# Optimization experiments

Measured on AMD Instinct MI355X. Metric: run time of the kernel, lower is better.

## Reference

```python
import jax, jax.numpy as jnp
import numpy as np

# dims: L layers, T steps, N envs, D d_model, H heads, DH d_head, M mem_len, DI d_inner
L, T, N, D, H, DH, M, DI = 6, 128, 32, 1024, 16, 64, 128, 4096


def _layer_norm(x, g, b, eps=1e-5):
    mu = jnp.mean(x, axis=-1, keepdims=True)
    var = jnp.mean(jnp.square(x - mu), axis=-1, keepdims=True)
    return (x - mu) * jax.lax.rsqrt(var + eps) * g + b


def _rel_shift(x):
    # x: (n, h, q, k) with k axis indexed by relative distance (k-1 .. 0)
    n, h, q, k = x.shape
    x = jnp.pad(x, ((0, 0), (0, 0), (0, 0), (1, 0)))
    x = x.reshape(n, h, k + 1, q)[:, :, 1:, :].reshape(n, h, q, k)
    return x


def setup_inputs() -> dict:
    key = jax.random.key(0)
    ks = jax.random.split(key, 16)
    s = 0.02
    inp = {
        "x": jax.random.normal(ks[0], (T * N, D), jnp.float32),
        "context": jax.random.normal(ks[1], (T * N, D), jnp.float32),
        "mems": jax.random.normal(ks[2], (L, N, M, D), jnp.float32),
        "masks": jnp.ones((T * N,), jnp.float32),
        "Wq": jax.random.normal(ks[3], (L, D, H * DH), jnp.float32) * s,
        "Wk": jax.random.normal(ks[4], (L, D, H * DH), jnp.float32) * s,
        "Wv": jax.random.normal(ks[5], (L, D, H * DH), jnp.float32) * s,
        "Wr": jax.random.normal(ks[6], (L, D, H * DH), jnp.float32) * s,
        "Wo": jax.random.normal(ks[7], (L, H * DH, D), jnp.float32) * s,
        "W1": jax.random.normal(ks[8], (L, D, DI), jnp.float32) * s,
        "b1": jnp.zeros((L, DI), jnp.float32),
        "W2": jax.random.normal(ks[9], (L, DI, D), jnp.float32) * s,
        "b2": jnp.zeros((L, D), jnp.float32),
        "ln1_g": jnp.ones((L, D), jnp.float32),
        "ln1_b": jnp.zeros((L, D), jnp.float32),
        "ln2_g": jnp.ones((L, D), jnp.float32),
        "ln2_b": jnp.zeros((L, D), jnp.float32),
        "r_w_bias": jax.random.normal(ks[10], (H, DH), jnp.float32) * s,
        "r_r_bias": jax.random.normal(ks[11], (H, DH), jnp.float32) * s,
    }
    return inp


def reference(x, context, mems, masks, Wq, Wk, Wv, Wr, Wo, W1, b1, W2, b2,
              ln1_g, ln1_b, ln2_g, ln2_b, r_w_bias, r_r_bias):
    n = mems.shape[1]
    t = x.shape[0] // n
    m = mems.shape[2]
    klen = m + t
    dh = r_w_bias.shape[-1]
    h_heads = r_w_bias.shape[0]

    xs = x.reshape(t, n, -1)
    ctx = context.reshape(t, n, -1)
    mk = masks.reshape(t, n)

    # zero memories for envs that reset at the first step (mems * masks)
    mems = mems * mk[0][None, :, None, None]

    # episode-reset attention mask: token i attends token j iff j<=i and no
    # reset (mask==0) happened between them; memory visible only before any reset
    ep = jnp.cumsum((mk == 0.0).astype(jnp.int32), axis=0)  # (t, n)
    epT = ep.T  # (n, t)
    causal = jnp.tril(jnp.ones((t, t), bool))
    allow_seq = causal[None, :, :] & (epT[:, :, None] == epT[:, None, :])  # (n,t,t)
    allow_mem = jnp.broadcast_to((epT == 0)[:, :, None], (n, t, m))  # (n,t,m)
    allow = jnp.concatenate([allow_mem, allow_seq], axis=-1)[:, None]  # (n,1,t,K)

    # sinusoidal relative position embedding, distances klen-1 .. 0
    pos = jnp.arange(klen - 1, -1, -1, dtype=x.dtype)
    inv_freq = 1.0 / (10000.0 ** (jnp.arange(0, xs.shape[-1], 2, dtype=x.dtype) / xs.shape[-1]))
    ang = pos[:, None] * inv_freq[None, :]
    R = jnp.concatenate([jnp.sin(ang), jnp.cos(ang)], axis=-1)  # (K, D)

    h = xs + ctx  # fuse observation features with goal context
    scale = 1.0 / jnp.sqrt(jnp.asarray(dh, x.dtype))

    n_layer = mems.shape[0]
    for l in range(n_layer):
        cat = jnp.concatenate([jnp.transpose(mems[l], (1, 0, 2)), h], axis=0)  # (K,n,D)
        q = (h @ Wq[l]).reshape(t, n, h_heads, dh)
        k = (cat @ Wk[l]).reshape(klen, n, h_heads, dh)
        v = (cat @ Wv[l]).reshape(klen, n, h_heads, dh)
        r = (R @ Wr[l]).reshape(klen, h_heads, dh)
        AC = jnp.einsum('inhd,jnhd->nhij', q + r_w_bias, k)
        BD = _rel_shift(jnp.einsum('inhd,jhd->nhij', q + r_r_bias, r))
        score = (AC + BD) * scale
        score = jnp.where(allow, score, -1e9)
        attn = jax.nn.softmax(score, axis=-1)
        o = jnp.einsum('nhij,jnhd->inhd', attn, v).reshape(t, n, h_heads * dh) @ Wo[l]
        h = _layer_norm(h + o, ln1_g[l], ln1_b[l])
        f = jax.nn.relu(h @ W1[l] + b1[l]) @ W2[l] + b2[l]
        h = _layer_norm(h + f, ln2_g[l], ln2_b[l])

    return h.reshape(t * n, -1)
```

## Files before the change

### kernel.cpp

```cpp
#include <hip/hip_runtime.h>
#include <stdint.h>

#define DEV static __device__ __forceinline__

typedef __attribute__((ext_vector_type(4))) float f32x4;
typedef __attribute__((ext_vector_type(8))) short bf16x8;
typedef __attribute__((ext_vector_type(4))) short s16x4;

static constexpr int L_ = 6, T_ = 128, NE = 32, D_ = 1024, H_ = 16, DH_ = 64, M_ = 128, DI_ = 4096;
static constexpr int KLEN = M_ + T_;
static constexpr int TN = T_ * NE;
static constexpr int NB = NE * H_;

DEV unsigned short f2bf(float f) {
  unsigned u = __builtin_bit_cast(unsigned, f);
  u += 0x7FFFu + ((u >> 16) & 1u);
  return (unsigned short)(u >> 16);
}
DEV float bf2f(unsigned short h) {
  unsigned u = ((unsigned)h) << 16;
  return __builtin_bit_cast(float, u);
}

DEV void gload16(const unsigned short* g, unsigned short* lds) {
  __builtin_amdgcn_global_load_lds(
      (const __attribute__((address_space(1))) unsigned int*)g,
      (__attribute__((address_space(3))) unsigned int*)lds, 16, 0, 0);
}

DEV void stage128(const unsigned short* __restrict__ Ab, int lda,
                  const unsigned short* __restrict__ Bb, int ldb,
                  unsigned short* lA, unsigned short* lB,
                  int m0, int n0, int k0, int w, int l)
{
#pragma unroll
  for (int i = 0; i < 4; ++i) {
    const int obb = i * 4096 + w * 1024;
    const int ob  = obb + (l << 4);
    const int row = ob >> 7;
    const int col = (((ob >> 4) & 7) ^ (row & 7)) << 3;
    gload16(Ab + (size_t)(m0 + row) * lda + k0 + col, lA + (obb >> 1));
    gload16(Bb + (size_t)(n0 + row) * ldb + k0 + col, lB + (obb >> 1));
  }
}

DEV void compute128(const unsigned short* lA, const unsigned short* lB,
                    int w, int l, f32x4 acc[4][4])
{
  const int wr = (w >> 1) * 64, wc = (w & 1) * 64;
  const int lan = l & 15, lgr = l >> 4;
#pragma unroll
  for (int ks = 0; ks < 2; ++ks) {
    bf16x8 av[4], bv[4];
#pragma unroll
    for (int m = 0; m < 4; ++m) {
      const int row = wr + m * 16 + lan;
      const int byte = ((row << 7) + (ks << 6) + (lgr << 4)) ^ ((row & 7) << 4);
      av[m] = *(const bf16x8*)((const char*)lA + byte);
    }
#pragma unroll
    for (int n = 0; n < 4; ++n) {
      const int row = wc + n * 16 + lan;
      const int byte = ((row << 7) + (ks << 6) + (lgr << 4)) ^ ((row & 7) << 4);
      bv[n] = *(const bf16x8*)((const char*)lB + byte);
    }
#pragma unroll
    for (int m = 0; m < 4; ++m)
#pragma unroll
      for (int n = 0; n < 4; ++n)
        acc[m][n] = __builtin_amdgcn_mfma_f32_16x16x32_bf16(av[m], bv[n], acc[m][n], 0, 0, 0);
  }
}

DEV void gemm128_2ph(const unsigned short* __restrict__ Ab, int lda,
                     const unsigned short* __restrict__ Bb, int ldb,
                     unsigned short (*shA)[8192], unsigned short (*shB)[8192],
                     int m0, int n0, int nK, int w, int l, f32x4 acc[4][4])
{
  stage128(Ab, lda, Bb, ldb, shA[0], shB[0], m0, n0, 0, w, l);
  asm volatile("s_waitcnt vmcnt(0)" ::: "memory");
  __syncthreads();
  int cur = 0;
  for (int kt = 0; kt < nK; ++kt) {
    if (kt + 1 < nK)
      stage128(Ab, lda, Bb, ldb, shA[cur ^ 1], shB[cur ^ 1], m0, n0, (kt + 1) * 64, w, l);
    compute128(shA[cur], shB[cur], w, l, acc);
    asm volatile("s_waitcnt vmcnt(0)" ::: "memory");
    __syncthreads();
    cur ^= 1;
  }
}

template <int EPI>
__global__ __launch_bounds__(256) void gemm_bt(
    const unsigned short* __restrict__ A, int lda, int sAn, int sAh,
    const unsigned short* __restrict__ B, int ldb, int sBn, int sBh,
    void* __restrict__ Cv, int ldc, int sC,
    const float* __restrict__ bias, int nK, int Hb)
{
  __shared__ unsigned short shA[2][8192];
  __shared__ unsigned short shB[2][8192];

  const int z = blockIdx.z;
  const int bn = z / Hb, bh = z % Hb;
  const unsigned short* Ab = A + (size_t)bn * sAn + (size_t)bh * sAh;
  const unsigned short* Bb = B + (size_t)bn * sBn + (size_t)bh * sBh;
  const int m0 = blockIdx.y * 128;
  const int n0 = blockIdx.x * 128;

  const int t = threadIdx.x;
  const int w = t >> 6, l = t & 63;
  const int wr = (w >> 1) * 64, wc = (w & 1) * 64;
  const int lan = l & 15, lgr = l >> 4;

  f32x4 acc[4][4];
#pragma unroll
  for (int m = 0; m < 4; ++m)
#pragma unroll
    for (int n = 0; n < 4; ++n) acc[m][n] = (f32x4){0.f, 0.f, 0.f, 0.f};

  gemm128_2ph(Ab, lda, Bb, ldb, shA, shB, m0, n0, nK, w, l, acc);

  const int zc = z * sC;
#pragma unroll
  for (int m = 0; m < 4; ++m) {
    const int row = m0 + wr + m * 16 + lgr * 4;
#pragma unroll
    for (int n = 0; n < 4; ++n) {
      const int col = n0 + wc + n * 16 + lan;
      const float bcol = (EPI >= 2) ? bias[col] : 0.f;
#pragma unroll
      for (int e = 0; e < 4; ++e) {
        float v = acc[m][n][e];
        const size_t idx = (size_t)zc + (size_t)(row + e) * ldc + col;
        if (EPI == 0) {
          ((float*)Cv)[idx] = v;
        } else if (EPI == 1) {
          ((unsigned short*)Cv)[idx] = f2bf(v);
        } else if (EPI == 2) {
          v += bcol; v = v > 0.f ? v : 0.f;
          ((unsigned short*)Cv)[idx] = f2bf(v);
        } else {
          ((float*)Cv)[idx] = v + bcol;
        }
      }
    }
  }
}

__global__ __launch_bounds__(256) void gemm_proj(
    const unsigned short* __restrict__ catA, const unsigned short* __restrict__ wt,
    unsigned short* __restrict__ kb, unsigned short* __restrict__ vb,
    unsigned short* __restrict__ qw, unsigned short* __restrict__ qr,
    unsigned short* __restrict__ rb,
    const float* __restrict__ rwb, const float* __restrict__ rrb)
{
  __shared__ unsigned short shA[2][8192];
  __shared__ unsigned short shB[2][8192];

  const int id = blockIdx.x;
  int by, bx;
  if (id < 1024)      { by = id >> 4;               bx = id & 15; }
  else if (id < 1280) { const int u = id - 1024; by = 32 + (u >> 3); bx = 16 + (u & 7); }
  else                { const int u = id - 1280; by = 64 + (u >> 3); bx = 24 + (u & 7); }
  const int m0 = by * 128, n0 = bx * 128;

  const int t = threadIdx.x;
  const int w = t >> 6, l = t & 63;
  const int wr = (w >> 1) * 64, wc = (w & 1) * 64;
  const int lan = l & 15, lgr = l >> 4;

  f32x4 acc[4][4];
#pragma unroll
  for (int m = 0; m < 4; ++m)
#pragma unroll
    for (int n = 0; n < 4; ++n) acc[m][n] = (f32x4){0.f, 0.f, 0.f, 0.f};

  gemm128_2ph(catA, 1024, wt, 1024, shA, shB, m0, n0, 16, w, l, acc);

#pragma unroll
  for (int m = 0; m < 4; ++m) {
    const int row = m0 + wr + m * 16 + lgr * 4;
#pragma unroll
    for (int n = 0; n < 4; ++n) {
      const int col = n0 + wc + n * 16 + lan;
#pragma unroll
      for (int e = 0; e < 4; ++e) {
        const float v = acc[m][n][e];
        const int r = row + e;
        if (col < 1024) {
          kb[(size_t)r * 1024 + col] = f2bf(v);
        } else if (col < 2048) {
          vb[(size_t)r * 1024 + col - 1024] = f2bf(v);
        } else if (col < 3072) {
          const int c = col - 2048;
          const size_t o = (size_t)(r - 4096) * 1024 + c;
          qw[o] = f2bf(v + rwb[c]);
          qr[o] = f2bf(v + rrb[c]);
        } else {
          const int c = col - 3072;
          rb[(size_t)(r - 8192) * 1024 + c] = f2bf(v);
        }
      }
    }
  }
}

__global__ __launch_bounds__(256) void gemm_scores(
    const unsigned short* __restrict__ qw, const unsigned short* __restrict__ qr,
    const unsigned short* __restrict__ kbf, const unsigned short* __restrict__ rbf,
    unsigned short* __restrict__ AC, unsigned short* __restrict__ BD)
{
  __shared__ unsigned short shA[2][8192];
  __shared__ unsigned short shB[2][8192];

  const int bx = blockIdx.x;
  const int z = blockIdx.y;
  const int nn = z >> 4, hh = z & 15;
  const bool isBD = bx >= 2;
  const int n0 = (bx & 1) * 128;
  const unsigned short* Ab = (isBD ? qr : qw) + (size_t)nn * 1024 + hh * 64;
  const unsigned short* Bb = isBD ? (rbf + hh * 64)
                                  : (kbf + (size_t)nn * 1024 + hh * 64);
  const int ldb = isBD ? 1024 : (NE * 1024);
  unsigned short* C = (isBD ? BD : AC) + (size_t)z * (T_ * KLEN);

  const int t = threadIdx.x;
  const int w = t >> 6, l = t & 63;
  const int wr = (w >> 1) * 64, wc = (w & 1) * 64;
  const int lan = l & 15, lgr = l >> 4;

  f32x4 acc[4][4];
#pragma unroll
  for (int m = 0; m < 4; ++m)
#pragma unroll
    for (int n = 0; n < 4; ++n) acc[m][n] = (f32x4){0.f, 0.f, 0.f, 0.f};

  gemm128_2ph(Ab, NE * 1024, Bb, ldb, shA, shB, 0, n0, 1, w, l, acc);

#pragma unroll
  for (int m = 0; m < 4; ++m) {
    const int row = wr + m * 16 + lgr * 4;
#pragma unroll
    for (int n = 0; n < 4; ++n) {
      const int col = n0 + wc + n * 16 + lan;
#pragma unroll
      for (int e = 0; e < 4; ++e)
        C[(size_t)(row + e) * KLEN + col] = f2bf(acc[m][n][e]);
    }
  }
}

__global__ __launch_bounds__(256) void pv_kernel(
    const unsigned short* __restrict__ P, const unsigned short* __restrict__ V,
    unsigned short* __restrict__ O)
{
  const int z = blockIdx.x;
  const int nn = z >> 4, hh = z & 15;
  const int t = threadIdx.x, w = t >> 6, l = t & 63;
  const int lan = l & 15, lgr = l >> 4;
  const int i0 = w * 32;
  const unsigned short* Pz = P + (size_t)z * (T_ * KLEN);
  const unsigned short* Vz = V + hh * DH_;

  f32x4 acc[2][4];
#pragma unroll
  for (int m = 0; m < 2; ++m)
#pragma unroll
    for (int n = 0; n < 4; ++n) acc[m][n] = (f32x4){0.f, 0.f, 0.f, 0.f};

  for (int ks = 0; ks < 8; ++ks) {
    const int kb = ks * 32 + lgr * 8;
    bf16x8 bv[4];
#pragma unroll
    for (int n = 0; n < 4; ++n) {
      const int d = n * 16 + lan;
      bf16x8 tmp;
#pragma unroll
      for (int jj = 0; jj < 8; ++jj)
        tmp[jj] = (short)Vz[(size_t)((kb + jj) * NE + nn) * 1024 + d];
      bv[n] = tmp;
    }
    bf16x8 av[2];
#pragma unroll
    for (int m = 0; m < 2; ++m)
      av[m] = *(const bf16x8*)&Pz[(size_t)(i0 + m * 16 + lan) * KLEN + kb];
#pragma unroll
    for (int m = 0; m < 2; ++m)
#pragma unroll
      for (int n = 0; n < 4; ++n)
        acc[m][n] = __builtin_amdgcn_mfma_f32_16x16x32_bf16(av[m], bv[n], acc[m][n], 0, 0, 0);
  }
#pragma unroll
  for (int m = 0; m < 2; ++m)
#pragma unroll
    for (int n = 0; n < 4; ++n)
#pragma unroll
      for (int e = 0; e < 4; ++e) {
        const int i = i0 + m * 16 + lgr * 4 + e;
        const int d = n * 16 + lan;
        O[(size_t)(i * NE + nn) * 1024 + hh * DH_ + d] = f2bf(acc[m][n][e]);
      }
}

__global__ __launch_bounds__(256) void softmax_kernel(
    const unsigned short* __restrict__ AC, const unsigned short* __restrict__ BD,
    const int* __restrict__ ep, unsigned short* __restrict__ P)
{
  const int g = blockIdx.x * 4 + (threadIdx.x >> 6);
  const int l = threadIdx.x & 63;
  const int z = g >> 7, i = g & 127;
  const int nn = z >> 4;
  const size_t base = (size_t)z * (T_ * KLEN) + (size_t)i * KLEN;
  const int j0 = l * 4;
  const int epi = ep[i * NE + nn];
  s16x4 ac4 = *(const s16x4*)&AC[base + j0];
  float sc[4];
#pragma unroll
  for (int q = 0; q < 4; ++q) {
    const int j = j0 + q;
    int jx = j + (T_ - 1) - i; if (jx > KLEN - 1) jx = KLEN - 1;
    const float bd = bf2f((unsigned short)BD[base + jx]);
    bool allow;
    if (j < M_) {
      allow = (epi == 0);
    } else {
      const int jp = j - M_;
      allow = (jp <= i) && (ep[jp * NE + nn] == epi);
    }
    const float v = (bf2f((unsigned short)ac4[q]) + bd) * 0.125f;
    sc[q] = allow ? v : -1e9f;
  }
  float mx = fmaxf(fmaxf(sc[0], sc[1]), fmaxf(sc[2], sc[3]));
#pragma unroll
  for (int o = 32; o; o >>= 1) mx = fmaxf(mx, __shfl_xor(mx, o));
  float p[4], sum = 0.f;
#pragma unroll
  for (int q = 0; q < 4; ++q) { p[q] = __expf(sc[q] - mx); sum += p[q]; }
#pragma unroll
  for (int o = 32; o; o >>= 1) sum += __shfl_xor(sum, o);
  const float inv = 1.f / sum;
  s16x4 o4;
#pragma unroll
  for (int q = 0; q < 4; ++q) o4[q] = (short)f2bf(p[q] * inv);
  *(s16x4*)&P[base + j0] = o4;
}

__global__ __launch_bounds__(256) void transpose_kernel(
    const float* __restrict__ W, unsigned short* __restrict__ WT, int Kd, int Nd)
{
  __shared__ float tile[32][33];
  const int tx = threadIdx.x & 31, ty = threadIdx.x >> 5;
  const int nIn = blockIdx.x * 32 + tx;
  const int kBase = blockIdx.y * 32;
#pragma unroll
  for (int r = 0; r < 32; r += 8)
    tile[ty + r][tx] = W[(size_t)(kBase + ty + r) * Nd + nIn];
  __syncthreads();
#pragma unroll
  for (int r = 0; r < 32; r += 8)
    WT[(size_t)(blockIdx.x * 32 + ty + r) * Kd + kBase + tx] = f2bf(tile[tx][ty + r]);
}

__global__ __launch_bounds__(256) void catmem_kernel(
    const float* __restrict__ mems_l, const float* __restrict__ masks,
    unsigned short* __restrict__ cat)
{
  const int idx = blockIdx.x * 256 + threadIdx.x;
  const int d = idx & 1023;
  const int r = idx >> 10;
  const int nn = r & 31, j = r >> 5;
  const float mk0 = masks[nn];
  cat[idx] = f2bf(mems_l[(size_t)(nn * M_ + j) * 1024 + d] * mk0);
}

__global__ __launch_bounds__(256) void hprep_kernel(
    const float* __restrict__ x, const float* __restrict__ ctx,
    float* __restrict__ h, unsigned short* __restrict__ catUp)
{
  const int idx = blockIdx.x * 256 + threadIdx.x;
  const float v = x[idx] + ctx[idx];
  h[idx] = v;
  catUp[idx] = f2bf(v);
}

__global__ __launch_bounds__(256) void rpos_kernel(unsigned short* __restrict__ R)
{
  const int idx = blockIdx.x * 256 + threadIdx.x;
  const int d = idx & 1023, j = idx >> 10;
  const float pos = (float)(KLEN - 1 - j);
  const int f = d & 511;
  const float inv_freq = __expf(-((float)(2 * f) * (1.f / 1024.f)) * 9.210340371976184f);
  const float ang = pos * inv_freq;
  const float v = (d < 512) ? sinf(ang) : cosf(ang);
  R[idx] = f2bf(v);
}

__global__ void ep_kernel(const float* __restrict__ masks, int* __restrict__ ep)
{
  const int nn = threadIdx.x;
  if (nn < NE) {
    int c = 0;
    for (int i = 0; i < T_; ++i) {
      c += (masks[i * NE + nn] == 0.f) ? 1 : 0;
      ep[i * NE + nn] = c;
    }
  }
}

__global__ __launch_bounds__(256) void ln_kernel(
    const float* __restrict__ a, const float* __restrict__ p0,
    const float* __restrict__ p1, const float* __restrict__ bias,
    const float* __restrict__ g, const float* __restrict__ bb,
    float* __restrict__ outf, unsigned short* __restrict__ outbf)
{
  const int row = blockIdx.x;
  const int t = threadIdx.x, w = t >> 6, l = t & 63;
  const int c = t * 4;
  const size_t base = (size_t)row * 1024;
  f32x4 va = *(const f32x4*)&a[base + c];
  f32x4 v0 = *(const f32x4*)&p0[base + c];
  f32x4 v1 = *(const f32x4*)&p1[base + c];
  f32x4 v = va + v0 + v1;
  if (bias) {
    f32x4 vb = *(const f32x4*)&bias[c];
    v = v + vb;
  }
  float s = v[0] + v[1] + v[2] + v[3];
#pragma unroll
  for (int o = 32; o; o >>= 1) s += __shfl_xor(s, o);
  __shared__ float red[8];
  if (l == 0) red[w] = s;
  __syncthreads();
  s = red[0] + red[1] + red[2] + red[3];
  const float mu = s * (1.f / 1024.f);
  f32x4 dv = v - mu;
  float s2 = dv[0]*dv[0] + dv[1]*dv[1] + dv[2]*dv[2] + dv[3]*dv[3];
#pragma unroll
  for (int o = 32; o; o >>= 1) s2 += __shfl_xor(s2, o);
  if (l == 0) red[4 + w] = s2;
  __syncthreads();
  s2 = red[4] + red[5] + red[6] + red[7];
  const float inv = rsqrtf(s2 * (1.f / 1024.f) + 1e-5f);
  f32x4 y;
#pragma unroll
  for (int q = 0; q < 4; ++q) y[q] = dv[q] * inv * g[c + q] + bb[c + q];
  *(f32x4*)&outf[base + c] = y;
  if (outbf) {
    s16x4 o4;
#pragma unroll
    for (int q = 0; q < 4; ++q) o4[q] = (short)f2bf(y[q]);
    *(s16x4*)&outbf[base + c] = o4;
  }
}

extern "C" void kernel_launch(void* const* d_in, const int* in_sizes, int n_in,
                              void* d_out, int out_size, void* d_ws, size_t ws_size,
                              hipStream_t stream)
{
  (void)in_sizes; (void)n_in; (void)out_size; (void)ws_size;
  const float* x    = (const float*)d_in[0];
  const float* ctx  = (const float*)d_in[1];
  const float* mems = (const float*)d_in[2];
  const float* masks= (const float*)d_in[3];
  const float* Wq   = (const float*)d_in[4];
  const float* Wk   = (const float*)d_in[5];
  const float* Wv   = (const float*)d_in[6];
  const float* Wr   = (const float*)d_in[7];
  const float* Wo   = (const float*)d_in[8];
  const float* W1   = (const float*)d_in[9];
  const float* b1   = (const float*)d_in[10];
  const float* W2   = (const float*)d_in[11];
  const float* b2   = (const float*)d_in[12];
  const float* ln1g = (const float*)d_in[13];
  const float* ln1b = (const float*)d_in[14];
  const float* ln2g = (const float*)d_in[15];
  const float* ln2b = (const float*)d_in[16];
  const float* rwb  = (const float*)d_in[17];
  const float* rrb  = (const float*)d_in[18];

  char* ws = (char*)d_ws;
  size_t off = 0;
  auto alloc = [&](size_t bytes) {
    char* p = ws + off;
    off += (bytes + 255) & ~(size_t)255;
    return p;
  };
  unsigned short* wtAll = (unsigned short*)alloc(4096u * 1024 * 2);
  unsigned short* wto = (unsigned short*)alloc(1024u * 1024 * 2);
  unsigned short* wt1 = (unsigned short*)alloc(4096u * 1024 * 2);
  unsigned short* wt2 = (unsigned short*)alloc(4096u * 1024 * 2);
  unsigned short* cat = (unsigned short*)alloc((size_t)(KLEN * NE + 256) * 1024 * 2);
  unsigned short* rbf = (unsigned short*)alloc((size_t)KLEN * 1024 * 2);
  int*            epb = (int*)alloc((size_t)T_ * NE * 4);
  float*          h   = (float*)alloc((size_t)TN * 1024 * 4);
  float*          h1  = (float*)alloc((size_t)TN * 1024 * 4);
  unsigned short* qw  = (unsigned short*)alloc((size_t)TN * 1024 * 2);
  unsigned short* qr  = (unsigned short*)alloc((size_t)TN * 1024 * 2);
  unsigned short* kbf = (unsigned short*)alloc((size_t)KLEN * NE * 1024 * 2);
  unsigned short* vbf = (unsigned short*)alloc((size_t)KLEN * NE * 1024 * 2);
  unsigned short* ACb = (unsigned short*)alloc((size_t)NB * T_ * KLEN * 2);
  unsigned short* BDb = (unsigned short*)alloc((size_t)NB * T_ * KLEN * 2);
  unsigned short* Pb  = (unsigned short*)alloc((size_t)NB * T_ * KLEN * 2);
  unsigned short* obf = (unsigned short*)alloc((size_t)TN * 1024 * 2);

  unsigned short* wtk = wtAll;
  unsigned short* wtv = wtAll + 1024u * 1024;
  unsigned short* wtq = wtAll + 2u * 1024 * 1024;
  unsigned short* wtr = wtAll + 3u * 1024 * 1024;
  unsigned short* catUp = cat + (size_t)M_ * NE * 1024;
  unsigned short* catR  = cat + (size_t)KLEN * NE * 1024;
  unsigned short* f1 = ACb;
  float* part = (float*)BDb;
  float* part1 = part + (size_t)TN * 1024;
  unsigned short* h1bf = qw;

  rpos_kernel<<<KLEN * 1024 / 256, 256, 0, stream>>>(catR);
  ep_kernel<<<1, 64, 0, stream>>>(masks, epb);
  hprep_kernel<<<TN * 1024 / 256, 256, 0, stream>>>(x, ctx, h, catUp);

  for (int l = 0; l < L_; ++l) {
    const size_t wOff = (size_t)l * 1024 * 1024;
    const size_t wOffBig = (size_t)l * 1024 * 4096;
    transpose_kernel<<<dim3(32, 32), 256, 0, stream>>>(Wk + wOff, wtk, 1024, 1024);
    transpose_kernel<<<dim3(32, 32), 256, 0, stream>>>(Wv + wOff, wtv, 1024, 1024);
    transpose_kernel<<<dim3(32, 32), 256, 0, stream>>>(Wq + wOff, wtq, 1024, 1024);
    transpose_kernel<<<dim3(32, 32), 256, 0, stream>>>(Wr + wOff, wtr, 1024, 1024);
    transpose_kernel<<<dim3(32, 32), 256, 0, stream>>>(Wo + wOff, wto, 1024, 1024);
    transpose_kernel<<<dim3(128, 32), 256, 0, stream>>>(W1 + wOffBig, wt1, 1024, 4096);
    transpose_kernel<<<dim3(32, 128), 256, 0, stream>>>(W2 + wOffBig, wt2, 4096, 1024);
    catmem_kernel<<<M_ * NE * 1024 / 256, 256, 0, stream>>>(
        mems + (size_t)l * NE * M_ * 1024, masks, cat);

    gemm_proj<<<1296, 256, 0, stream>>>(cat, wtAll, kbf, vbf, qw, qr, rbf, rwb, rrb);

    gemm_scores<<<dim3(4, 512), 256, 0, stream>>>(qw, qr, kbf, rbf, ACb, BDb);

    softmax_kernel<<<NB * T_ / 4, 256, 0, stream>>>(ACb, BDb, epb, Pb);
    pv_kernel<<<NB, 256, 0, stream>>>(Pb, vbf, obf);

    gemm_bt<0><<<dim3(8, 32, 2), 256, 0, stream>>>(obf, 1024, 0, 512,
                                                   wto, 1024, 0, 512,
                                                   part, 1024, TN * 1024, nullptr, 8, 2);
    ln_kernel<<<TN, 256, 0, stream>>>(h, part, part1, nullptr,
                                      ln1g + l * 1024, ln1b + l * 1024, h1, h1bf);

    gemm_bt<2><<<dim3(32, 32, 1), 256, 0, stream>>>(h1bf, 1024, 0, 0, wt1, 1024, 0, 0,
                                                    f1, 4096, 0, b1 + l * 4096, 16, 1);
    gemm_bt<0><<<dim3(8, 32, 2), 256, 0, stream>>>(f1, 4096, 0, 2048,
                                                   wt2, 4096, 0, 2048,
                                                   part, 1024, TN * 1024, nullptr, 32, 2);
    ln_kernel<<<TN, 256, 0, stream>>>(h1, part, part1, b2 + l * 1024,
                                      ln2g + l * 1024, ln2b + l * 1024,
                                      (l == L_ - 1) ? (float*)d_out : h, catUp);
  }
}
```

Measured before the change: 1.939 ms.

## Switch dense GEMMs to 256x256 tiles with triple-buffered pipeline and split-K 4

Replaces the 128x128 double-buffered GEMMs with 256x256-tile, 512-thread kernels that keep three LDS stages of K=32 in flight, using partial vmcnt waits and raw barriers. The aim is more data reuse per tile and better overlap of loads with MFMA work. Split-K for the Wo and W2 GEMMs grows from 2 to 4 partials, so the layer-norm kernel now sums four partial buffers. The five square weight transposes are merged into one launch. Larger tiles mean fewer blocks for the projection GEMM and higher register and LDS pressure, and the extra partials add memory traffic.

```diff
diff --git a/kernel.cpp b/kernel.cpp
--- a/kernel.cpp
+++ b/kernel.cpp
@@ -2,6 +2,7 @@
 #include <stdint.h>
 
 #define DEV static __device__ __forceinline__
+typedef unsigned short ushort_t;
 
 typedef __attribute__((ext_vector_type(4))) float f32x4;
 typedef __attribute__((ext_vector_type(8))) short bf16x8;
@@ -28,162 +29,168 @@
       (__attribute__((address_space(3))) unsigned int*)lds, 16, 0, 0);
 }
 
-DEV void stage128(const unsigned short* __restrict__ Ab, int lda,
+#define WAITV8 asm volatile("s_waitcnt vmcnt(8)" ::: "memory")
+#define WAITV4 asm volatile("s_waitcnt vmcnt(4)" ::: "memory")
+#define WAITV0 asm volatile("s_waitcnt vmcnt(0)" ::: "memory")
+#define BARRAW asm volatile("s_barrier" ::: "memory")
+
+DEV void stage256(const unsigned short* __restrict__ Ab, int lda,
                   const unsigned short* __restrict__ Bb, int ldb,
                   unsigned short* lA, unsigned short* lB,
-                  int m0, int n0, int k0, int w, int l)
-{
-#pragma unroll
-  for (int i = 0; i < 4; ++i) {
-    const int obb = i * 4096 + w * 1024;
+                  int m0, int n0, int k0, int t)
+{
+  const int w = t >> 6, l = t & 63;
+#pragma unroll
+  for (int r = 0; r < 2; ++r) {
+    const int obb = r * 8192 + w * 1024;
     const int ob  = obb + (l << 4);
-    const int row = ob >> 7;
-    const int col = (((ob >> 4) & 7) ^ (row & 7)) << 3;
+    const int row = ob >> 6;
+    const int p   = (ob >> 4) & 3;
+    const int col = ((p ^ row ^ (row >> 2)) & 3) << 3;
     gload16(Ab + (size_t)(m0 + row) * lda + k0 + col, lA + (obb >> 1));
+  }
+#pragma unroll
+  for (int r = 0; r < 2; ++r) {
+    const int obb = r * 8192 + w * 1024;
+    const int ob  = obb + (l << 4);
+    const int row = ob >> 6;
+    const int p   = (ob >> 4) & 3;
+    const int col = ((p ^ row ^ (row >> 2)) & 3) << 3;
     gload16(Bb + (size_t)(n0 + row) * ldb + k0 + col, lB + (obb >> 1));
   }
 }
 
-DEV void compute128(const unsigned short* lA, const unsigned short* lB,
-                    int w, int l, f32x4 acc[4][4])
-{
-  const int wr = (w >> 1) * 64, wc = (w & 1) * 64;
+DEV void compute256(const unsigned short* lA, const unsigned short* lB,
+                    int w, int l, f32x4 acc[8][4])
+{
+  const int wm = w >> 2, wn = w & 3;
   const int lan = l & 15, lgr = l >> 4;
-#pragma unroll
-  for (int ks = 0; ks < 2; ++ks) {
-    bf16x8 av[4], bv[4];
-#pragma unroll
-    for (int m = 0; m < 4; ++m) {
-      const int row = wr + m * 16 + lan;
-      const int byte = ((row << 7) + (ks << 6) + (lgr << 4)) ^ ((row & 7) << 4);
-      av[m] = *(const bf16x8*)((const char*)lA + byte);
-    }
+  bf16x8 av[8], bv[4];
+#pragma unroll
+  for (int m = 0; m < 8; ++m) {
+    const int row = wm * 128 + m * 16 + lan;
+    const int p = (lgr ^ row ^ (row >> 2)) & 3;
+    av[m] = *(const bf16x8*)((const char*)lA + row * 64 + p * 16);
+  }
+#pragma unroll
+  for (int n = 0; n < 4; ++n) {
+    const int row = wn * 64 + n * 16 + lan;
+    const int p = (lgr ^ row ^ (row >> 2)) & 3;
+    bv[n] = *(const bf16x8*)((const char*)lB + row * 64 + p * 16);
+  }
+  __builtin_amdgcn_s_setprio(1);
+#pragma unroll
+  for (int m = 0; m < 8; ++m)
+#pragma unroll
+    for (int n = 0; n < 4; ++n)
+      acc[m][n] = __builtin_amdgcn_mfma_f32_16x16x32_bf16(av[m], bv[n], acc[m][n], 0, 0, 0);
+  __builtin_amdgcn_s_setprio(0);
+}
+
+DEV void gemm256_pipe(const unsigned short* __restrict__ Ab, int lda,
+                      const unsigned short* __restrict__ Bb, int ldb,
+                      unsigned short (*sA)[8192], unsigned short (*sB)[8192],
+                      int m0, int n0, int nK, int t, f32x4 acc[8][4])
+{
+  stage256(Ab, lda, Bb, ldb, sA[0], sB[0], m0, n0, 0, t);
+  if (nK > 1) stage256(Ab, lda, Bb, ldb, sA[1], sB[1], m0, n0, 32, t);
+  if (nK > 2) stage256(Ab, lda, Bb, ldb, sA[2], sB[2], m0, n0, 64, t);
+  const int w = t >> 6, l = t & 63;
+  int buf = 0;
+  for (int kt = 0; kt < nK; ++kt) {
+    if (kt + 2 < nK)      { WAITV8; }
+    else if (kt + 1 < nK) { WAITV4; }
+    else                  { WAITV0; }
+    BARRAW;
+    compute256(sA[buf], sB[buf], w, l, acc);
+    BARRAW;
+    if (kt + 3 < nK)
+      stage256(Ab, lda, Bb, ldb, sA[buf], sB[buf], m0, n0, (kt + 3) * 32, t);
+    buf = (buf == 2) ? 0 : buf + 1;
+  }
+}
+
+template <int EPI>
+__global__ __launch_bounds__(512, 2) void gemm256_bt(
+    const unsigned short* __restrict__ A, int lda, int sAh,
+    const unsigned short* __restrict__ B, int ldb, int sBh,
+    void* __restrict__ Cv, int ldc, int sC,
+    const float* __restrict__ bias, int nK)
+{
+  __shared__ unsigned short sA[3][8192];
+  __shared__ unsigned short sB[3][8192];
+  const int z = blockIdx.z;
+  const unsigned short* Ab = A + (size_t)z * sAh;
+  const unsigned short* Bb = B + (size_t)z * sBh;
+  const int m0 = blockIdx.y * 256, n0 = blockIdx.x * 256;
+  const int t = threadIdx.x;
+
+  f32x4 acc[8][4];
+#pragma unroll
+  for (int m = 0; m < 8; ++m)
+#pragma unroll
+    for (int n = 0; n < 4; ++n) acc[m][n] = (f32x4){0.f, 0.f, 0.f, 0.f};
+
+  gemm256_pipe(Ab, lda, Bb, ldb, sA, sB, m0, n0, nK, t, acc);
+
+  const int w = t >> 6, l = t & 63;
+  const int wm = w >> 2, wn = w & 3, lan = l & 15, lgr = l >> 4;
+  const size_t zc = (size_t)z * sC;
+#pragma unroll
+  for (int m = 0; m < 8; ++m) {
+    const int row = m0 + wm * 128 + m * 16 + lgr * 4;
 #pragma unroll
     for (int n = 0; n < 4; ++n) {
-      const int row = wc + n * 16 + lan;
-      const int byte = ((row << 7) + (ks << 6) + (lgr << 4)) ^ ((row & 7) << 4);
-      bv[n] = *(const bf16x8*)((const char*)lB + byte);
-    }
-#pragma unroll
-    for (int m = 0; m < 4; ++m)
-#pragma unroll
-      for (int n = 0; n < 4; ++n)
-        acc[m][n] = __builtin_amdgcn_mfma_f32_16x16x32_bf16(av[m], bv[n], acc[m][n], 0, 0, 0);
-  }
-}
-
-DEV void gemm128_2ph(const unsigned short* __restrict__ Ab, int lda,
-                     const unsigned short* __restrict__ Bb, int ldb,
-                     unsigned short (*shA)[8192], unsigned short (*shB)[8192],
-                     int m0, int n0, int nK, int w, int l, f32x4 acc[4][4])
-{
-  stage128(Ab, lda, Bb, ldb, shA[0], shB[0], m0, n0, 0, w, l);
-  asm volatile("s_waitcnt vmcnt(0)" ::: "memory");
-  __syncthreads();
-  int cur = 0;
-  for (int kt = 0; kt < nK; ++kt) {
-    if (kt + 1 < nK)
-      stage128(Ab, lda, Bb, ldb, shA[cur ^ 1], shB[cur ^ 1], m0, n0, (kt + 1) * 64, w, l);
-    compute128(shA[cur], shB[cur], w, l, acc);
-    asm volatile("s_waitcnt vmcnt(0)" ::: "memory");
-    __syncthreads();
-    cur ^= 1;
-  }
-}
-
-template <int EPI>
-__global__ __launch_bounds__(256) void gemm_bt(
-    const unsigned short* __restrict__ A, int lda, int sAn, int sAh,
-    const unsigned short* __restrict__ B, int ldb, int sBn, int sBh,
-    void* __restrict__ Cv, int ldc, int sC,
-    const float* __restrict__ bias, int nK, int Hb)
-{
-  __shared__ unsigned short shA[2][8192];
-  __shared__ unsigned short shB[2][8192];
-
-  const int z = blockIdx.z;
-  const int bn = z / Hb, bh = z % Hb;
-  const unsigned short* Ab = A + (size_t)bn * sAn + (size_t)bh * sAh;
-  const unsigned short* Bb = B + (size_t)bn * sBn + (size_t)bh * sBh;
-  const int m0 = blockIdx.y * 128;
-  const int n0 = blockIdx.x * 128;
-
-  const int t = threadIdx.x;
-  const int w = t >> 6, l = t & 63;
-  const int wr = (w >> 1) * 64, wc = (w & 1) * 64;
-  const int lan = l & 15, lgr = l >> 4;
-
-  f32x4 acc[4][4];
-#pragma unroll
-  for (int m = 0; m < 4; ++m)
-#pragma unroll
-    for (int n = 0; n < 4; ++n) acc[m][n] = (f32x4){0.f, 0.f, 0.f, 0.f};
-
-  gemm128_2ph(Ab, lda, Bb, ldb, shA, shB, m0, n0, nK, w, l, acc);
-
-  const int zc = z * sC;
-#pragma unroll
-  for (int m = 0; m < 4; ++m) {
-    const int row = m0 + wr + m * 16 + lgr * 4;
-#pragma unroll
-    for (int n = 0; n < 4; ++n) {
-      const int col = n0 + wc + n * 16 + lan;
+      const int col = n0 + wn * 64 + n * 16 + lan;
       const float bcol = (EPI >= 2) ? bias[col] : 0.f;
 #pragma unroll
       for (int e = 0; e < 4; ++e) {
         float v = acc[m][n][e];
-        const size_t idx = (size_t)zc + (size_t)(row + e) * ldc + col;
+        const size_t idx = zc + (size_t)(row + e) * ldc + col;
         if (EPI == 0) {
           ((float*)Cv)[idx] = v;
-        } else if (EPI == 1) {
-          ((unsigned short*)Cv)[idx] = f2bf(v);
-        } else if (EPI == 2) {
+        } else {
           v += bcol; v = v > 0.f ? v : 0.f;
           ((unsigned short*)Cv)[idx] = f2bf(v);
-        } else {
-          ((float*)Cv)[idx] = v + bcol;
         }
       }
     }
   }
 }
 
-__global__ __launch_bounds__(256) void gemm_proj(
+__global__ __launch_bounds__(512, 2) void gemm256_proj(
     const unsigned short* __restrict__ catA, const unsigned short* __restrict__ wt,
     unsigned short* __restrict__ kb, unsigned short* __restrict__ vb,
     unsigned short* __restrict__ qw, unsigned short* __restrict__ qr,
     unsigned short* __restrict__ rb,
     const float* __restrict__ rwb, const float* __restrict__ rrb)
 {
-  __shared__ unsigned short shA[2][8192];
-  __shared__ unsigned short shB[2][8192];
-
+  __shared__ unsigned short sA[3][8192];
+  __shared__ unsigned short sB[3][8192];
   const int id = blockIdx.x;
   int by, bx;
-  if (id < 1024)      { by = id >> 4;               bx = id & 15; }
-  else if (id < 1280) { const int u = id - 1024; by = 32 + (u >> 3); bx = 16 + (u & 7); }
-  else                { const int u = id - 1280; by = 64 + (u >> 3); bx = 24 + (u & 7); }
-  const int m0 = by * 128, n0 = bx * 128;
-
+  if (id < 256)      { by = id >> 3;                 bx = id & 7; }
+  else if (id < 320) { const int u = id - 256; by = 16 + (u >> 2); bx = 8 + (u & 3); }
+  else               { const int u = id - 320; by = 32;            bx = 12 + (u & 3); }
+  const int m0 = by * 256, n0 = bx * 256;
   const int t = threadIdx.x;
+
+  f32x4 acc[8][4];
+#pragma unroll
+  for (int m = 0; m < 8; ++m)
+#pragma unroll
+    for (int n = 0; n < 4; ++n) acc[m][n] = (f32x4){0.f, 0.f, 0.f, 0.f};
+
+  gemm256_pipe(catA, 1024, wt, 1024, sA, sB, m0, n0, 32, t, acc);
+
   const int w = t >> 6, l = t & 63;
-  const int wr = (w >> 1) * 64, wc = (w & 1) * 64;
-  const int lan = l & 15, lgr = l >> 4;
-
-  f32x4 acc[4][4];
-#pragma unroll
-  for (int m = 0; m < 4; ++m)
-#pragma unroll
-    for (int n = 0; n < 4; ++n) acc[m][n] = (f32x4){0.f, 0.f, 0.f, 0.f};
-
-  gemm128_2ph(catA, 1024, wt, 1024, shA, shB, m0, n0, 16, w, l, acc);
-
-#pragma unroll
-  for (int m = 0; m < 4; ++m) {
-    const int row = m0 + wr + m * 16 + lgr * 4;
+  const int wm = w >> 2, wn = w & 3, lan = l & 15, lgr = l >> 4;
+#pragma unroll
+  for (int m = 0; m < 8; ++m) {
+    const int row = m0 + wm * 128 + m * 16 + lgr * 4;
 #pragma unroll
     for (int n = 0; n < 4; ++n) {
-      const int col = n0 + wc + n * 16 + lan;
+      const int col = n0 + wn * 64 + n * 16 + lan;
 #pragma unroll
       for (int e = 0; e < 4; ++e) {
         const float v = acc[m][n][e];
@@ -206,13 +213,57 @@
   }
 }
 
+DEV void stage128(const unsigned short* __restrict__ Ab, int lda,
+                  const unsigned short* __restrict__ Bb, int ldb,
+                  unsigned short* lA, unsigned short* lB,
+                  int m0, int n0, int k0, int w, int l)
+{
+#pragma unroll
+  for (int i = 0; i < 4; ++i) {
+    const int obb = i * 4096 + w * 1024;
+    const int ob  = obb + (l << 4);
+    const int row = ob >> 7;
+    const int col = (((ob >> 4) & 7) ^ (row & 7)) << 3;
+    gload16(Ab + (size_t)(m0 + row) * lda + k0 + col, lA + (obb >> 1));
+    gload16(Bb + (size_t)(n0 + row) * ldb + k0 + col, lB + (obb >> 1));
+  }
+}
+
+DEV void compute128(const unsigned short* lA, const unsigned short* lB,
+                    int w, int l, f32x4 acc[4][4])
+{
+  const int wr = (w >> 1) * 64, wc = (w & 1) * 64;
+  const int lan = l & 15, lgr = l >> 4;
+#pragma unroll
+  for (int ks = 0; ks < 2; ++ks) {
+    bf16x8 av[4], bv[4];
+#pragma unroll
+    for (int m = 0; m < 4; ++m) {
+      const int row = wr + m * 16 + lan;
+      const int byte = ((row << 7) + (ks << 6) + (lgr << 4)) ^ ((row & 7) << 4);
+      av[m] = *(const bf16x8*)((const char*)lA + byte);
+    }
+#pragma unroll
+    for (int n = 0; n < 4; ++n) {
+      const int row = wc + n * 16 + lan;
+      const int byte = ((row << 7) + (ks << 6) + (lgr << 4)) ^ ((row & 7) << 4);
+      bv[n] = *(const bf16x8*)((const char*)lB + byte);
+    }
+#pragma unroll
+    for (int m = 0; m < 4; ++m)
+#pragma unroll
+      for (int n = 0; n < 4; ++n)
+        acc[m][n] = __builtin_amdgcn_mfma_f32_16x16x32_bf16(av[m], bv[n], acc[m][n], 0, 0, 0);
+  }
+}
+
 __global__ __launch_bounds__(256) void gemm_scores(
     const unsigned short* __restrict__ qw, const unsigned short* __restrict__ qr,
     const unsigned short* __restrict__ kbf, const unsigned short* __restrict__ rbf,
     unsigned short* __restrict__ AC, unsigned short* __restrict__ BD)
 {
-  __shared__ unsigned short shA[2][8192];
-  __shared__ unsigned short shB[2][8192];
+  __shared__ unsigned short shA[8192];
+  __shared__ unsigned short shB[8192];
 
   const int bx = blockIdx.x;
   const int z = blockIdx.y;
@@ -236,7 +287,10 @@
 #pragma unroll
     for (int n = 0; n < 4; ++n) acc[m][n] = (f32x4){0.f, 0.f, 0.f, 0.f};
 
-  gemm128_2ph(Ab, NE * 1024, Bb, ldb, shA, shB, 0, n0, 1, w, l, acc);
+  stage128(Ab, NE * 1024, Bb, ldb, shA, shB, 0, n0, 0, w, l);
+  asm volatile("s_waitcnt vmcnt(0)" ::: "memory");
+  __syncthreads();
+  compute128(shA, shB, w, l, acc);
 
 #pragma unroll
   for (int m = 0; m < 4; ++m) {
@@ -362,6 +416,28 @@
     WT[(size_t)(blockIdx.x * 32 + ty + r) * Kd + kBase + tx] = f2bf(tile[tx][ty + r]);
 }
 
+__global__ __launch_bounds__(256) void transpose5_kernel(
+    const float* __restrict__ Wk, const float* __restrict__ Wv,
+    const float* __restrict__ Wq, const float* __restrict__ Wr,
+    const float* __restrict__ Wo,
+    unsigned short* __restrict__ wtAll, unsigned short* __restrict__ wto)
+{
+  __shared__ float tile[32][33];
+  const int zz = blockIdx.z;
+  const float* W = (zz == 0) ? Wk : (zz == 1) ? Wv : (zz == 2) ? Wq : (zz == 3) ? Wr : Wo;
+  unsigned short* WT = (zz == 4) ? wto : (wtAll + (size_t)zz * 1024 * 1024);
+  const int tx = threadIdx.x & 31, ty = threadIdx.x >> 5;
+  const int nIn = blockIdx.x * 32 + tx;
+  const int kBase = blockIdx.y * 32;
+#pragma unroll
+  for (int r = 0; r < 32; r += 8)
+    tile[ty + r][tx] = W[(size_t)(kBase + ty + r) * 1024 + nIn];
+  __syncthreads();
+#pragma unroll
+  for (int r = 0; r < 32; r += 8)
+    WT[(size_t)(blockIdx.x * 32 + ty + r) * 1024 + kBase + tx] = f2bf(tile[tx][ty + r]);
+}
+
 __global__ __launch_bounds__(256) void catmem_kernel(
     const float* __restrict__ mems_l, const float* __restrict__ masks,
     unsigned short* __restrict__ cat)
@@ -410,7 +486,8 @@
 
 __global__ __launch_bounds__(256) void ln_kernel(
     const float* __restrict__ a, const float* __restrict__ p0,
-    const float* __restrict__ p1, const float* __restrict__ bias,
+    const float* __restrict__ p1, const float* __restrict__ p2,
+    const float* __restrict__ p3, const float* __restrict__ bias,
     const float* __restrict__ g, const float* __restrict__ bb,
     float* __restrict__ outf, unsigned short* __restrict__ outbf)
 {
@@ -418,14 +495,12 @@
   const int t = threadIdx.x, w = t >> 6, l = t & 63;
   const int c = t * 4;
   const size_t base = (size_t)row * 1024;
-  f32x4 va = *(const f32x4*)&a[base + c];
-  f32x4 v0 = *(const f32x4*)&p0[base + c];
-  f32x4 v1 = *(const f32x4*)&p1[base + c];
-  f32x4 v = va + v0 + v1;
-  if (bias) {
-    f32x4 vb = *(const f32x4*)&bias[c];
-    v = v + vb;
-  }
+  f32x4 v = *(const f32x4*)&a[base + c];
+  v = v + *(const f32x4*)&p0[base + c];
+  v = v + *(const f32x4*)&p1[base + c];
+  v = v + *(const f32x4*)&p2[base + c];
+  v = v + *(const f32x4*)&p3[base + c];
+  if (bias) v = v + *(const f32x4*)&bias[c];
   float s = v[0] + v[1] + v[2] + v[3];
 #pragma unroll
   for (int o = 32; o; o >>= 1) s += __shfl_xor(s, o);
@@ -504,15 +579,10 @@
   unsigned short* Pb  = (unsigned short*)alloc((size_t)NB * T_ * KLEN * 2);
   unsigned short* obf = (unsigned short*)alloc((size_t)TN * 1024 * 2);
 
-  unsigned short* wtk = wtAll;
-  unsigned short* wtv = wtAll + 1024u * 1024;
-  unsigned short* wtq = wtAll + 2u * 1024 * 1024;
-  unsigned short* wtr = wtAll + 3u * 1024 * 1024;
   unsigned short* catUp = cat + (size_t)M_ * NE * 1024;
   unsigned short* catR  = cat + (size_t)KLEN * NE * 1024;
   unsigned short* f1 = ACb;
   float* part = (float*)BDb;
-  float* part1 = part + (size_t)TN * 1024;
   unsigned short* h1bf = qw;
 
   rpos_kernel<<<KLEN * 1024 / 256, 256, 0, stream>>>(catR);
@@ -522,36 +592,36 @@
   for (int l = 0; l < L_; ++l) {
     const size_t wOff = (size_t)l * 1024 * 1024;
     const size_t wOffBig = (size_t)l * 1024 * 4096;
-    transpose_kernel<<<dim3(32, 32), 256, 0, stream>>>(Wk + wOff, wtk, 1024, 1024);
-    transpose_kernel<<<dim3(32, 32), 256, 0, stream>>>(Wv + wOff, wtv, 1024, 1024);
-    transpose_kernel<<<dim3(32, 32), 256, 0, stream>>>(Wq + wOff, wtq, 1024, 1024);
-    transpose_kernel<<<dim3(32, 32), 256, 0, stream>>>(Wr + wOff, wtr, 1024, 1024);
-    transpose_kernel<<<dim3(32, 32), 256, 0, stream>>>(Wo + wOff, wto, 1024, 1024);
+    transpose5_kernel<<<dim3(32, 32, 5), 256, 0, stream>>>(
+        Wk + wOff, Wv + wOff, Wq + wOff, Wr + wOff, Wo + wOff, wtAll, wto);
     transpose_kernel<<<dim3(128, 32), 256, 0, stream>>>(W1 + wOffBig, wt1, 1024, 4096);
     transpose_kernel<<<dim3(32, 128), 256, 0, stream>>>(W2 + wOffBig, wt2, 4096, 1024);
     catmem_kernel<<<M_ * NE * 1024 / 256, 256, 0, stream>>>(
         mems + (size_t)l * NE * M_ * 1024, masks, cat);
 
-    gemm_proj<<<1296, 256, 0, stream>>>(cat, wtAll, kbf, vbf, qw, qr, rbf, rwb, rrb);
+    gemm256_proj<<<324, 512, 0, stream>>>(cat, wtAll, kbf, vbf, qw, qr, rbf, rwb, rrb);
 
     gemm_scores<<<dim3(4, 512), 256, 0, stream>>>(qw, qr, kbf, rbf, ACb, BDb);
 
     softmax_kernel<<<NB * T_ / 4, 256, 0, stream>>>(ACb, BDb, epb, Pb);
     pv_kernel<<<NB, 256, 0, stream>>>(Pb, vbf, obf);
 
-    gemm_bt<0><<<dim3(8, 32, 2), 256, 0, stream>>>(obf, 1024, 0, 512,
-                                                   wto, 1024, 0, 512,
-                                                   part, 1024, TN * 1024, nullptr, 8, 2);
-    ln_kernel<<<TN, 256, 0, stream>>>(h, part, part1, nullptr,
-                                      ln1g + l * 1024, ln1b + l * 1024, h1, h1bf);
-
-    gemm_bt<2><<<dim3(32, 32, 1), 256, 0, stream>>>(h1bf, 1024, 0, 0, wt1, 1024, 0, 0,
-                                                    f1, 4096, 0, b1 + l * 4096, 16, 1);
-    gemm_bt<0><<<dim3(8, 32, 2), 256, 0, stream>>>(f1, 4096, 0, 2048,
-                                                   wt2, 4096, 0, 2048,
-                                                   part, 1024, TN * 1024, nullptr, 32, 2);
-    ln_kernel<<<TN, 256, 0, stream>>>(h1, part, part1, b2 + l * 1024,
-                                      ln2g + l * 1024, ln2b + l * 1024,
+    gemm256_bt<0><<<dim3(4, 16, 4), 512, 0, stream>>>(
+        obf, 1024, 256, wto, 1024, 256,
+        part, 1024, TN * 1024, nullptr, 8);
+    ln_kernel<<<TN, 256, 0, stream>>>(h, part, part + (size_t)TN * 1024,
+                                      part + (size_t)2 * TN * 1024, part + (size_t)3 * TN * 1024,
+                                      nullptr, ln1g + l * 1024, ln1b + l * 1024, h1, h1bf);
+
+    gemm256_bt<2><<<dim3(16, 16, 1), 512, 0, stream>>>(
+        h1bf, 1024, 0, wt1, 1024, 0,
+        f1, 4096, 0, b1 + l * 4096, 32);
+    gemm256_bt<0><<<dim3(4, 16, 4), 512, 0, stream>>>(
+        f1, 4096, 1024, wt2, 4096, 1024,
+        part, 1024, TN * 1024, nullptr, 32);
+    ln_kernel<<<TN, 256, 0, stream>>>(h1, part, part + (size_t)TN * 1024,
+                                      part + (size_t)2 * TN * 1024, part + (size_t)3 * TN * 1024,
+                                      b2 + l * 1024, ln2g + l * 1024, ln2b + l * 1024,
                                       (l == L_ - 1) ? (float*)d_out : h, catUp);
   }
 }
```

Result: slower. 2.319 ms (+19.6%).

## Fuse softmax into PV kernel via LDS and batch five weight transposes

Applied to the files above, without the earlier changes.

The softmax over attention scores is now computed inside the PV kernel. Each block writes its 128x256 probability tile into XOR-swizzled shared memory instead of a global P buffer, and the MFMA loop reads it back from there. This removes a full bf16 P round trip through HBM and one kernel launch per layer. The five 1024x1024 weight transposes are also merged into one launch with a z-dimension. The trade-off is a 64KB LDS allocation per block, which limits occupancy, and a serial 32-row softmax loop per wave before the matmul starts.

```diff
diff --git a/kernel.cpp b/kernel.cpp
--- a/kernel.cpp
+++ b/kernel.cpp
@@ -251,16 +251,59 @@
   }
 }
 
-__global__ __launch_bounds__(256) void pv_kernel(
-    const unsigned short* __restrict__ P, const unsigned short* __restrict__ V,
+__global__ __launch_bounds__(256) void smpv_kernel(
+    const unsigned short* __restrict__ AC, const unsigned short* __restrict__ BD,
+    const int* __restrict__ ep, const unsigned short* __restrict__ V,
     unsigned short* __restrict__ O)
 {
+  __shared__ unsigned short sP[128 * 256];
+
   const int z = blockIdx.x;
   const int nn = z >> 4, hh = z & 15;
   const int t = threadIdx.x, w = t >> 6, l = t & 63;
   const int lan = l & 15, lgr = l >> 4;
+  const size_t zbase = (size_t)z * (T_ * KLEN);
+
+  const int j0 = l * 4;
+  for (int rr = 0; rr < 32; ++rr) {
+    const int i = w * 32 + rr;
+    const int epi = ep[i * NE + nn];
+    const size_t base = zbase + (size_t)i * KLEN;
+    s16x4 ac4 = *(const s16x4*)&AC[base + j0];
+    float sc[4];
+#pragma unroll
+    for (int q = 0; q < 4; ++q) {
+      const int j = j0 + q;
+      int jx = j + (T_ - 1) - i; if (jx > KLEN - 1) jx = KLEN - 1;
+      const float bd = bf2f((unsigned short)BD[base + jx]);
+      bool allow;
+      if (j < M_) {
+        allow = (epi == 0);
+      } else {
+        const int jp = j - M_;
+        allow = (jp <= i) && (ep[jp * NE + nn] == epi);
+      }
+      const float v = (bf2f((unsigned short)ac4[q]) + bd) * 0.125f;
+      sc[q] = allow ? v : -1e9f;
+    }
+    float mx = fmaxf(fmaxf(sc[0], sc[1]), fmaxf(sc[2], sc[3]));
+#pragma unroll
+    for (int o = 32; o; o >>= 1) mx = fmaxf(mx, __shfl_xor(mx, o));
+    float p[4], sum = 0.f;
+#pragma unroll
+    for (int q = 0; q < 4; ++q) { p[q] = __expf(sc[q] - mx); sum += p[q]; }
+#pragma unroll
+    for (int o = 32; o; o >>= 1) sum += __shfl_xor(sum, o);
+    const float inv = 1.f / sum;
+    s16x4 o4;
+#pragma unroll
+    for (int q = 0; q < 4; ++q) o4[q] = (short)f2bf(p[q] * inv);
+    const int swz = ((i >> 2) & 3) * 16;
+    *(s16x4*)&sP[i * 256 + (j0 ^ swz)] = o4;
+  }
+  __syncthreads();
+
   const int i0 = w * 32;
-  const unsigned short* Pz = P + (size_t)z * (T_ * KLEN);
   const unsigned short* Vz = V + hh * DH_;
 
   f32x4 acc[2][4];
@@ -283,8 +326,11 @@
     }
     bf16x8 av[2];
 #pragma unroll
-    for (int m = 0; m < 2; ++m)
-      av[m] = *(const bf16x8*)&Pz[(size_t)(i0 + m * 16 + lan) * KLEN + kb];
+    for (int m = 0; m < 2; ++m) {
+      const int row = i0 + m * 16 + lan;
+      const int swz = ((row >> 2) & 3) * 16;
+      av[m] = *(const bf16x8*)&sP[row * 256 + (kb ^ swz)];
+    }
 #pragma unroll
     for (int m = 0; m < 2; ++m)
 #pragma unroll
@@ -303,49 +349,6 @@
       }
 }
 
-__global__ __launch_bounds__(256) void softmax_kernel(
-    const unsigned short* __restrict__ AC, const unsigned short* __restrict__ BD,
-    const int* __restrict__ ep, unsigned short* __restrict__ P)
-{
-  const int g = blockIdx.x * 4 + (threadIdx.x >> 6);
-  const int l = threadIdx.x & 63;
-  const int z = g >> 7, i = g & 127;
-  const int nn = z >> 4;
-  const size_t base = (size_t)z * (T_ * KLEN) + (size_t)i * KLEN;
-  const int j0 = l * 4;
-  const int epi = ep[i * NE + nn];
-  s16x4 ac4 = *(const s16x4*)&AC[base + j0];
-  float sc[4];
-#pragma unroll
-  for (int q = 0; q < 4; ++q) {
-    const int j = j0 + q;
-    int jx = j + (T_ - 1) - i; if (jx > KLEN - 1) jx = KLEN - 1;
-    const float bd = bf2f((unsigned short)BD[base + jx]);
-    bool allow;
-    if (j < M_) {
-      allow = (epi == 0);
-    } else {
-      const int jp = j - M_;
-      allow = (jp <= i) && (ep[jp * NE + nn] == epi);
-    }
-    const float v = (bf2f((unsigned short)ac4[q]) + bd) * 0.125f;
-    sc[q] = allow ? v : -1e9f;
-  }
-  float mx = fmaxf(fmaxf(sc[0], sc[1]), fmaxf(sc[2], sc[3]));
-#pragma unroll
-  for (int o = 32; o; o >>= 1) mx = fmaxf(mx, __shfl_xor(mx, o));
-  float p[4], sum = 0.f;
-#pragma unroll
-  for (int q = 0; q < 4; ++q) { p[q] = __expf(sc[q] - mx); sum += p[q]; }
-#pragma unroll
-  for (int o = 32; o; o >>= 1) sum += __shfl_xor(sum, o);
-  const float inv = 1.f / sum;
-  s16x4 o4;
-#pragma unroll
-  for (int q = 0; q < 4; ++q) o4[q] = (short)f2bf(p[q] * inv);
-  *(s16x4*)&P[base + j0] = o4;
-}
-
 __global__ __launch_bounds__(256) void transpose_kernel(
     const float* __restrict__ W, unsigned short* __restrict__ WT, int Kd, int Nd)
 {
@@ -360,6 +363,28 @@
 #pragma unroll
   for (int r = 0; r < 32; r += 8)
     WT[(size_t)(blockIdx.x * 32 + ty + r) * Kd + kBase + tx] = f2bf(tile[tx][ty + r]);
+}
+
+__global__ __launch_bounds__(256) void transpose5_kernel(
+    const float* __restrict__ Wk, const float* __restrict__ Wv,
+    const float* __restrict__ Wq, const float* __restrict__ Wr,
+    const float* __restrict__ Wo,
+    unsigned short* __restrict__ wtAll, unsigned short* __restrict__ wto)
+{
+  __shared__ float tile[32][33];
+  const int zz = blockIdx.z;
+  const float* W = (zz == 0) ? Wk : (zz == 1) ? Wv : (zz == 2) ? Wq : (zz == 3) ? Wr : Wo;
+  unsigned short* WT = (zz == 4) ? wto : (wtAll + (size_t)zz * 1024 * 1024);
+  const int tx = threadIdx.x & 31, ty = threadIdx.x >> 5;
+  const int nIn = blockIdx.x * 32 + tx;
+  const int kBase = blockIdx.y * 32;
+#pragma unroll
+  for (int r = 0; r < 32; r += 8)
+    tile[ty + r][tx] = W[(size_t)(kBase + ty + r) * 1024 + nIn];
+  __syncthreads();
+#pragma unroll
+  for (int r = 0; r < 32; r += 8)
+    WT[(size_t)(blockIdx.x * 32 + ty + r) * 1024 + kBase + tx] = f2bf(tile[tx][ty + r]);
 }
 
 __global__ __launch_bounds__(256) void catmem_kernel(
@@ -501,13 +526,8 @@
   unsigned short* vbf = (unsigned short*)alloc((size_t)KLEN * NE * 1024 * 2);
   unsigned short* ACb = (unsigned short*)alloc((size_t)NB * T_ * KLEN * 2);
   unsigned short* BDb = (unsigned short*)alloc((size_t)NB * T_ * KLEN * 2);
-  unsigned short* Pb  = (unsigned short*)alloc((size_t)NB * T_ * KLEN * 2);
   unsigned short* obf = (unsigned short*)alloc((size_t)TN * 1024 * 2);
 
-  unsigned short* wtk = wtAll;
-  unsigned short* wtv = wtAll + 1024u * 1024;
-  unsigned short* wtq = wtAll + 2u * 1024 * 1024;
-  unsigned short* wtr = wtAll + 3u * 1024 * 1024;
   unsigned short* catUp = cat + (size_t)M_ * NE * 1024;
   unsigned short* catR  = cat + (size_t)KLEN * NE * 1024;
   unsigned short* f1 = ACb;
@@ -522,11 +542,8 @@
   for (int l = 0; l < L_; ++l) {
     const size_t wOff = (size_t)l * 1024 * 1024;
     const size_t wOffBig = (size_t)l * 1024 * 4096;
-    transpose_kernel<<<dim3(32, 32), 256, 0, stream>>>(Wk + wOff, wtk, 1024, 1024);
-    transpose_kernel<<<dim3(32, 32), 256, 0, stream>>>(Wv + wOff, wtv, 1024, 1024);
-    transpose_kernel<<<dim3(32, 32), 256, 0, stream>>>(Wq + wOff, wtq, 1024, 1024);
-    transpose_kernel<<<dim3(32, 32), 256, 0, stream>>>(Wr + wOff, wtr, 1024, 1024);
-    transpose_kernel<<<dim3(32, 32), 256, 0, stream>>>(Wo + wOff, wto, 1024, 1024);
+    transpose5_kernel<<<dim3(32, 32, 5), 256, 0, stream>>>(
+        Wk + wOff, Wv + wOff, Wq + wOff, Wr + wOff, Wo + wOff, wtAll, wto);
     transpose_kernel<<<dim3(128, 32), 256, 0, stream>>>(W1 + wOffBig, wt1, 1024, 4096);
     transpose_kernel<<<dim3(32, 128), 256, 0, stream>>>(W2 + wOffBig, wt2, 4096, 1024);
     catmem_kernel<<<M_ * NE * 1024 / 256, 256, 0, stream>>>(
@@ -536,8 +553,7 @@
 
     gemm_scores<<<dim3(4, 512), 256, 0, stream>>>(qw, qr, kbf, rbf, ACb, BDb);
 
-    softmax_kernel<<<NB * T_ / 4, 256, 0, stream>>>(ACb, BDb, epb, Pb);
-    pv_kernel<<<NB, 256, 0, stream>>>(Pb, vbf, obf);
+    smpv_kernel<<<NB, 256, 0, stream>>>(ACb, BDb, epb, vbf, obf);
 
     gemm_bt<0><<<dim3(8, 32, 2), 256, 0, stream>>>(obf, 1024, 0, 512,
                                                    wto, 1024, 0, 512,
```

New measurement: 1.945 ms. Within noise of the previous version (+0.3%).
